# Optimization experiments

Hardware: AMD Instinct MI355X
Metric: run time of the kernel (lower is better)

## Reference

```python
import jax, jax.numpy as jnp
import numpy as np

EMB = 1024
HEADS = 16
HEAD_DIM = EMB // HEADS
FF = 4 * EMB
EPS = 1e-5


def setup_inputs() -> dict:
    key = jax.random.key(0)
    ks = jax.random.split(key, 16)
    s = 0.02
    return {
        "x": jax.random.normal(ks[0], (2, 2048, EMB), dtype=jnp.float32),
        "ln1_g": jnp.ones((EMB,), jnp.float32),
        "ln1_b": jnp.zeros((EMB,), jnp.float32),
        "Wq": jax.random.normal(ks[1], (EMB, EMB), jnp.float32) * s,
        "bq": jnp.zeros((EMB,), jnp.float32),
        "Wk": jax.random.normal(ks[2], (EMB, EMB), jnp.float32) * s,
        "bk": jnp.zeros((EMB,), jnp.float32),
        "Wv": jax.random.normal(ks[3], (EMB, EMB), jnp.float32) * s,
        "bv": jnp.zeros((EMB,), jnp.float32),
        "Wo": jax.random.normal(ks[4], (EMB, EMB), jnp.float32) * s,
        "bo": jnp.zeros((EMB,), jnp.float32),
        "ln2_g": jnp.ones((EMB,), jnp.float32),
        "ln2_b": jnp.zeros((EMB,), jnp.float32),
        "W1": jax.random.normal(ks[5], (EMB, FF), jnp.float32) * s,
        "b1": jnp.zeros((FF,), jnp.float32),
        "W2": jax.random.normal(ks[6], (FF, EMB), jnp.float32) * s,
        "b2": jnp.zeros((EMB,), jnp.float32),
    }


def _layernorm(x, g, b):
    mu = jnp.mean(x, axis=-1, keepdims=True)
    var = jnp.var(x, axis=-1, keepdims=True)
    return (x - mu) * jax.lax.rsqrt(var + EPS) * g + b


def _attention(x, Wq, bq, Wk, bk, Wv, bv, Wo, bo):
    B, T, C = x.shape
    # [B,T,C] -> [B,H,T,Dh]
    def split(y):
        return y.reshape(B, T, HEADS, HEAD_DIM).transpose(0, 2, 1, 3)
    Q = split(x @ Wq + bq)
    K = split(x @ Wk + bk)
    V = split(x @ Wv + bv)
    att = jnp.einsum("bhqd,bhkd->bhqk", Q, K) / np.sqrt(HEAD_DIM).astype(np.float32)
    causal = jnp.tril(jnp.ones((T, T), bool))
    att = jnp.where(causal, att, -jnp.inf)
    att = jax.nn.softmax(att, axis=-1)
    out = jnp.einsum("bhqk,bhkd->bhqd", att, V)
    out = out.transpose(0, 2, 1, 3).reshape(B, T, C)
    return out @ Wo + bo


def reference(x, ln1_g, ln1_b, Wq, bq, Wk, bk, Wv, bv, Wo, bo,
              ln2_g, ln2_b, W1, b1, W2, b2):
    # dropout is identity in eval mode
    x = x + _attention(_layernorm(x, ln1_g, ln1_b), Wq, bq, Wk, bk, Wv, bv, Wo, bo)
    h = _layernorm(x, ln2_g, ln2_b)
    h = jax.nn.gelu(h @ W1 + b1, approximate=False) @ W2 + b2
    return x + h
```

## Files before the change

kernel.cpp:

```cpp
#include <hip/hip_runtime.h>
#include <hip/hip_bf16.h>

typedef __attribute__((ext_vector_type(4))) float f32x4;
typedef __attribute__((ext_vector_type(8))) short bf16x8;
typedef unsigned int u32;
typedef unsigned short u16;

#define GASP __attribute__((address_space(1)))
#define LASP __attribute__((address_space(3)))

__device__ __forceinline__ u16 f2bf(float f) {
  u32 u = __float_as_uint(f);
  return (u16)((u + 0x7fffu + ((u >> 16) & 1u)) >> 16);
}

__device__ __forceinline__ void gl_lds16(const void* g, void* l) {
  __builtin_amdgcn_global_load_lds((const GASP u32*)g, (LASP u32*)l, 16, 0, 0);
}

struct CastArgs {
  const float* s[6];
  u16* d[6];
};

__global__ __launch_bounds__(256) void cast_w(CastArgs a) {
  int bid = blockIdx.x;
  int w, t, K, N, kshift;
  if (bid < 4096)      { w = bid >> 10; t = bid & 1023; K = 1024; N = 1024; kshift = 5; }
  else if (bid < 8192) { w = 4; t = bid - 4096; K = 1024; N = 4096; kshift = 5; }
  else                 { w = 5; t = bid - 8192; K = 4096; N = 1024; kshift = 7; }
  int tk = t & ((1 << kshift) - 1);
  int tn = t >> kshift;
  int k0 = tk << 5, n0 = tn << 5;
  const float* src = a.s[w];
  u16* dst = a.d[w];
  __shared__ u16 tile[32][36];
  int r = threadIdx.x >> 3, c0 = (threadIdx.x & 7) << 2;
  float4 v = *(const float4*)&src[(size_t)(k0 + r) * N + n0 + c0];
  tile[c0 + 0][r] = f2bf(v.x);
  tile[c0 + 1][r] = f2bf(v.y);
  tile[c0 + 2][r] = f2bf(v.z);
  tile[c0 + 3][r] = f2bf(v.w);
  __syncthreads();
  ushort4 o;
  o.x = tile[r][c0 + 0];
  o.y = tile[r][c0 + 1];
  o.z = tile[r][c0 + 2];
  o.w = tile[r][c0 + 3];
  *(ushort4*)&dst[(size_t)(n0 + r) * K + k0 + c0] = o;
}

__global__ __launch_bounds__(256) void ln_k(const float* __restrict__ x, const float* __restrict__ g,
                                            const float* __restrict__ b, u16* __restrict__ out) {
  int row = blockIdx.x;
  int tid = threadIdx.x;
  float4 v = *(const float4*)&x[(size_t)row * 1024 + tid * 4];
  float s = v.x + v.y + v.z + v.w;
  float ss = v.x * v.x + v.y * v.y + v.z * v.z + v.w * v.w;
#pragma unroll
  for (int o = 32; o >= 1; o >>= 1) {
    s += __shfl_xor(s, o, 64);
    ss += __shfl_xor(ss, o, 64);
  }
  __shared__ float red[8];
  int wv = tid >> 6;
  if ((tid & 63) == 0) { red[wv] = s; red[wv + 4] = ss; }
  __syncthreads();
  s = red[0] + red[1] + red[2] + red[3];
  ss = red[4] + red[5] + red[6] + red[7];
  float mu = s * (1.0f / 1024.0f);
  float var = ss * (1.0f / 1024.0f) - mu * mu;
  float rstd = rsqrtf(var + 1e-5f);
  float4 gv = *(const float4*)&g[tid * 4];
  float4 bv = *(const float4*)&b[tid * 4];
  ushort4 o4;
  o4.x = f2bf((v.x - mu) * rstd * gv.x + bv.x);
  o4.y = f2bf((v.y - mu) * rstd * gv.y + bv.y);
  o4.z = f2bf((v.z - mu) * rstd * gv.z + bv.z);
  o4.w = f2bf((v.w - mu) * rstd * gv.w + bv.w);
  *(ushort4*)&out[(size_t)row * 1024 + tid * 4] = o4;
}

template <int MODE>
__global__ __launch_bounds__(512, 2) void gemm_256(
    const u16* __restrict__ A, const u16* __restrict__ Bt,
    const float* __restrict__ bias0, const float* __restrict__ bias1, const float* __restrict__ bias2,
    void* outp, int M, int N, int K) {
  __shared__ __align__(16) u16 As[3][256 * 32];
  __shared__ __align__(16) u16 Bs[3][256 * 32];
  const int tid = threadIdx.x;
  const int w = tid >> 6, lane = tid & 63;
  const int m0 = blockIdx.y << 8, n0 = blockIdx.x << 8;

  const u16* aS[2];
  const u16* bS[2];
  char* asB = (char*)As;
  char* bsB = (char*)Bs;
#pragma unroll
  for (int i = 0; i < 2; ++i) {
    int p = w * 2048 + i * 1024 + lane * 16;
    int r = p >> 6;
    int cl = ((p >> 4) & 3) ^ ((r >> 1) & 3);
    aS[i] = A + (size_t)(m0 + r) * K + cl * 8;
    bS[i] = Bt + (size_t)(n0 + r) * K + cl * 8;
  }
  f32x4 acc[8][4];
#pragma unroll
  for (int i = 0; i < 8; ++i)
#pragma unroll
    for (int j = 0; j < 4; ++j) acc[i][j] = f32x4{0.f, 0.f, 0.f, 0.f};

  const int wr = w >> 2, wc = w & 3;
  const int qi = lane & 15;
  int aOff[8], bOff[4];
#pragma unroll
  for (int mm = 0; mm < 8; ++mm) {
    int rowa = wr * 128 + mm * 16 + qi;
    aOff[mm] = rowa * 64 + (((lane >> 4) ^ ((rowa >> 1) & 3)) << 4);
  }
#pragma unroll
  for (int nn = 0; nn < 4; ++nn) {
    int rowb = wc * 64 + nn * 16 + qi;
    bOff[nn] = rowb * 64 + (((lane >> 4) ^ ((rowb >> 1) & 3)) << 4);
  }

  gl_lds16(aS[0], asB + w * 2048);
  gl_lds16(aS[1], asB + w * 2048 + 1024);
  gl_lds16(bS[0], bsB + w * 2048);
  gl_lds16(bS[1], bsB + w * 2048 + 1024);
  if (K > 32) {
    gl_lds16(aS[0] + 32, asB + 16384 + w * 2048);
    gl_lds16(aS[1] + 32, asB + 16384 + w * 2048 + 1024);
    gl_lds16(bS[0] + 32, bsB + 16384 + w * 2048);
    gl_lds16(bS[1] + 32, bsB + 16384 + w * 2048 + 1024);
  }
  int buf = 0;
  for (int ks = 0; ks < K; ks += 32) {
    if (ks + 32 >= K) { asm volatile("s_waitcnt vmcnt(0)" ::: "memory"); }
    else              { asm volatile("s_waitcnt vmcnt(4)" ::: "memory"); }
    __builtin_amdgcn_s_barrier();
    asm volatile("" ::: "memory");
    if (ks + 64 < K) {
      const int nb = ((buf + 2) % 3) * 16384;
      gl_lds16(aS[0] + ks + 64, asB + nb + w * 2048);
      gl_lds16(aS[1] + ks + 64, asB + nb + w * 2048 + 1024);
      gl_lds16(bS[0] + ks + 64, bsB + nb + w * 2048);
      gl_lds16(bS[1] + ks + 64, bsB + nb + w * 2048 + 1024);
    }
    const int tb = buf * 16384;
    bf16x8 av[8], bv[4];
#pragma unroll
    for (int mm = 0; mm < 8; ++mm) av[mm] = *(const bf16x8*)(asB + tb + aOff[mm]);
#pragma unroll
    for (int nn = 0; nn < 4; ++nn) bv[nn] = *(const bf16x8*)(bsB + tb + bOff[nn]);
    __builtin_amdgcn_s_setprio(1);
#pragma unroll
    for (int mm = 0; mm < 8; ++mm)
#pragma unroll
      for (int nn = 0; nn < 4; ++nn)
        acc[mm][nn] = __builtin_amdgcn_mfma_f32_16x16x32_bf16(av[mm], bv[nn], acc[mm][nn], 0, 0, 0);
    __builtin_amdgcn_s_setprio(0);
    buf = buf + 1;
    if (buf == 3) buf = 0;
  }

  const int g = lane >> 4, ci = lane & 15;
#pragma unroll
  for (int mm = 0; mm < 8; ++mm) {
#pragma unroll
    for (int nn = 0; nn < 4; ++nn) {
      int colb = n0 + wc * 64 + nn * 16 + ci;
      int rowbase = m0 + wr * 128 + mm * 16 + 4 * g;
      f32x4 c = acc[mm][nn];
      if constexpr (MODE == 2) {
        int sel = colb >> 10;
        int cc = colb & 1023;
        const float* bp = sel == 0 ? bias0 : (sel == 1 ? bias1 : bias2);
        float bb = bp[cc];
        int h = cc >> 6, d = cc & 63;
        int b_ = rowbase >> 11, tt = rowbase & 2047;
        if (sel == 2) {
          u16* op = (u16*)outp + 2ull * (4096ull * 1024ull);
          ushort4 o4;
          o4.x = f2bf(c[0] + bb);
          o4.y = f2bf(c[1] + bb);
          o4.z = f2bf(c[2] + bb);
          o4.w = f2bf(c[3] + bb);
          *(ushort4*)&op[((size_t)(b_ * 16 + h) * 64 + d) * 2048 + tt] = o4;
        } else {
          float scale = (sel == 0) ? 0.125f : 1.0f;
          u16* op = (u16*)outp + (size_t)sel * (4096ull * 1024ull);
#pragma unroll
          for (int r = 0; r < 4; ++r)
            op[((size_t)(b_ * 16 + h) * 2048 + tt + r) * 64 + d] = f2bf((c[r] + bb) * scale);
        }
      } else {
        float bb = bias0[colb];
#pragma unroll
        for (int r = 0; r < 4; ++r) {
          float v = c[r] + bb;
          float gl = 0.5f * v * (1.0f + erff(v * 0.70710678118654752f));
          ((u16*)outp)[(size_t)(rowbase + r) * N + colb] = f2bf(gl);
        }
      }
    }
  }
}

__global__ __launch_bounds__(512) void gemm_sk(
    const u16* __restrict__ A, const u16* __restrict__ Bt,
    const float* __restrict__ bias0, float* __restrict__ outp,
    const float* __restrict__ res, int M, int N, int K) {
  __shared__ __align__(16) union SM {
    struct { u16 As[2][3][128 * 32]; u16 Bs[2][3][128 * 32]; } t;
    float red[16][4][4][64];
  } sm;
  const int tid = threadIdx.x;
  const int w8 = tid >> 6, lane = tid & 63;
  const int gg = w8 >> 2, wl = w8 & 3;
  const int m0 = blockIdx.y << 7, n0 = blockIdx.x << 7;

  char* asB = (char*)sm.t.As[gg];
  char* bsB = (char*)sm.t.Bs[gg];
  const u16* aS[2];
  const u16* bS[2];
#pragma unroll
  for (int i = 0; i < 2; ++i) {
    int p = wl * 2048 + i * 1024 + lane * 16;
    int r = p >> 6;
    int cl = ((p >> 4) & 3) ^ ((r >> 1) & 3);
    aS[i] = A + (size_t)(m0 + r) * K + gg * 32 + cl * 8;
    bS[i] = Bt + (size_t)(n0 + r) * K + gg * 32 + cl * 8;
  }
  f32x4 acc[4][4];
#pragma unroll
  for (int i = 0; i < 4; ++i)
#pragma unroll
    for (int j = 0; j < 4; ++j) acc[i][j] = f32x4{0.f, 0.f, 0.f, 0.f};

  const int wr = wl >> 1, wc = wl & 1;
  int aOff[4], bOff[4];
#pragma unroll
  for (int mm = 0; mm < 4; ++mm) {
    int rowa = wr * 64 + mm * 16 + (lane & 15);
    aOff[mm] = rowa * 64 + (((lane >> 4) ^ ((rowa >> 1) & 3)) << 4);
    int rowb = wc * 64 + mm * 16 + (lane & 15);
    bOff[mm] = rowb * 64 + (((lane >> 4) ^ ((rowb >> 1) & 3)) << 4);
  }

  gl_lds16(aS[0], asB + wl * 2048);
  gl_lds16(aS[1], asB + wl * 2048 + 1024);
  gl_lds16(bS[0], bsB + wl * 2048);
  gl_lds16(bS[1], bsB + wl * 2048 + 1024);
  if (K > 64) {
    gl_lds16(aS[0] + 64, asB + 8192 + wl * 2048);
    gl_lds16(aS[1] + 64, asB + 8192 + wl * 2048 + 1024);
    gl_lds16(bS[0] + 64, bsB + 8192 + wl * 2048);
    gl_lds16(bS[1] + 64, bsB + 8192 + wl * 2048 + 1024);
  }
  int buf = 0;
  for (int ks = 0; ks < K; ks += 64) {
    if (ks + 64 >= K) { asm volatile("s_waitcnt vmcnt(0)" ::: "memory"); }
    else              { asm volatile("s_waitcnt vmcnt(4)" ::: "memory"); }
    __builtin_amdgcn_s_barrier();
    asm volatile("" ::: "memory");
    if (ks + 128 < K) {
      const int nb = ((buf + 2) % 3) * 8192;
      gl_lds16(aS[0] + ks + 128, asB + nb + wl * 2048);
      gl_lds16(aS[1] + ks + 128, asB + nb + wl * 2048 + 1024);
      gl_lds16(bS[0] + ks + 128, bsB + nb + wl * 2048);
      gl_lds16(bS[1] + ks + 128, bsB + nb + wl * 2048 + 1024);
    }
    const int tb = buf * 8192;
    bf16x8 av[4], bv[4];
#pragma unroll
    for (int mm = 0; mm < 4; ++mm) av[mm] = *(const bf16x8*)(asB + tb + aOff[mm]);
#pragma unroll
    for (int nn = 0; nn < 4; ++nn) bv[nn] = *(const bf16x8*)(bsB + tb + bOff[nn]);
#pragma unroll
    for (int mm = 0; mm < 4; ++mm)
#pragma unroll
      for (int nn = 0; nn < 4; ++nn)
        acc[mm][nn] = __builtin_amdgcn_mfma_f32_16x16x32_bf16(av[mm], bv[nn], acc[mm][nn], 0, 0, 0);
    buf = buf + 1;
    if (buf == 3) buf = 0;
  }

  __syncthreads();
  if (gg == 1) {
#pragma unroll
    for (int mm = 0; mm < 4; ++mm)
#pragma unroll
      for (int nn = 0; nn < 4; ++nn)
#pragma unroll
        for (int r = 0; r < 4; ++r) sm.red[mm * 4 + nn][r][wl][lane] = acc[mm][nn][r];
  }
  __syncthreads();
  if (gg == 0) {
    const int g = lane >> 4, ci = lane & 15;
#pragma unroll
    for (int mm = 0; mm < 4; ++mm) {
#pragma unroll
      for (int nn = 0; nn < 4; ++nn) {
        int colb = n0 + wc * 64 + nn * 16 + ci;
        int rowbase = m0 + wr * 64 + mm * 16 + 4 * g;
        float bb = bias0[colb];
#pragma unroll
        for (int r = 0; r < 4; ++r) {
          size_t idx = (size_t)(rowbase + r) * N + colb;
          outp[idx] = acc[mm][nn][r] + sm.red[mm * 4 + nn][r][wl][lane] + bb + res[idx];
        }
      }
    }
  }
}

__global__ __launch_bounds__(256) void attn_k(const u16* __restrict__ Q, const u16* __restrict__ Kg,
                                              const u16* __restrict__ Vt, u16* __restrict__ O) {
  __shared__ __align__(16) u16 Ks[2][64 * 64];
  __shared__ __align__(16) u16 Vs[2][64 * 64];
  const int bx = blockIdx.x;
  const int bh = blockIdx.y;
  const int tid = threadIdx.x, w = tid >> 6, lane = tid & 63;
  const int g = lane >> 4, qi = lane & 15;
  const u16* Qb = Q + (size_t)bh * 2048 * 64;
  const u16* Kb = Kg + (size_t)bh * 2048 * 64;
  const u16* Vtb = Vt + (size_t)bh * 64 * 2048;

  const int rl8 = lane >> 3;
  const int cs = ((lane & 7) ^ rl8) * 8;
  const u16* srcK0 = Kb + (size_t)(16 * w + rl8) * 64 + cs;
  const u16* srcK1 = srcK0 + 8 * 64;
  const u16* srcV0 = Vtb + (size_t)(16 * w + rl8) * 2048 + cs;
  const u16* srcV1 = srcV0 + 8 * 2048;
  char* ksB = (char*)Ks;
  char* vsB = (char*)Vs;
  const int dstOff = w * 2048 + lane * 16;

  int koff[4][2], voff[4][2];
#pragma unroll
  for (int t = 0; t < 4; ++t) {
    int row = 16 * t + qi;
#pragma unroll
    for (int h = 0; h < 2; ++h) koff[t][h] = row * 128 + (((4 * h + g) ^ (qi & 7)) << 4);
#pragma unroll
    for (int kt = 0; kt < 2; ++kt) voff[t][kt] = row * 128 + (((4 * kt + g) ^ (qi & 7)) << 4);
  }

  const int b_ = bh >> 4, hh = bh & 15;
  u32* Ou = (u32*)O;

  for (int job = 0; job < 2; ++job) {
    const int qt = job ? bx : 31 - bx;
    const int qrow = qt * 64 + w * 16 + qi;

    bf16x8 qf[2];
#pragma unroll
    for (int h = 0; h < 2; ++h)
      qf[h] = *(const bf16x8*)(Qb + (size_t)qrow * 64 + h * 32 + g * 8);

    f32x4 acc[4];
#pragma unroll
    for (int dt = 0; dt < 4; ++dt) acc[dt] = f32x4{0.f, 0.f, 0.f, 0.f};
    float m = -1e30f, lsum = 0.0f;

    __syncthreads();
    gl_lds16(srcK0, ksB + dstOff);
    gl_lds16(srcK1, ksB + dstOff + 1024);
    gl_lds16(srcV0, vsB + dstOff);
    gl_lds16(srcV1, vsB + dstOff + 1024);

    int buf = 0;
    for (int s = 0; s <= qt; ++s) {
      __syncthreads();
      if (s < qt) {
        int nb = buf ^ 1;
        gl_lds16(srcK0 + (size_t)(s + 1) * 4096, ksB + nb * 8192 + dstOff);
        gl_lds16(srcK1 + (size_t)(s + 1) * 4096, ksB + nb * 8192 + dstOff + 1024);
        gl_lds16(srcV0 + (size_t)(s + 1) * 64, vsB + nb * 8192 + dstOff);
        gl_lds16(srcV1 + (size_t)(s + 1) * 64, vsB + nb * 8192 + dstOff + 1024);
      }
      const int tb = buf * 8192;
      f32x4 st[4];
      __builtin_amdgcn_s_setprio(1);
#pragma unroll
      for (int t = 0; t < 4; ++t) {
        st[t] = f32x4{0.f, 0.f, 0.f, 0.f};
#pragma unroll
        for (int h = 0; h < 2; ++h) {
          bf16x8 kf = *(const bf16x8*)(ksB + tb + koff[t][h]);
          st[t] = __builtin_amdgcn_mfma_f32_16x16x32_bf16(kf, qf[h], st[t], 0, 0, 0);
        }
      }
      __builtin_amdgcn_s_setprio(0);
      float pvv[4][4];
      float tmax = -1e30f;
      if (s == qt) {
#pragma unroll
        for (int t = 0; t < 4; ++t)
#pragma unroll
          for (int r = 0; r < 4; ++r) {
            int key = 64 * s + 16 * t + 4 * g + r;
            float sv = st[t][r];
            sv = (key <= qrow) ? sv : -1e30f;
            pvv[t][r] = sv;
            tmax = fmaxf(tmax, sv);
          }
      } else {
#pragma unroll
        for (int t = 0; t < 4; ++t)
#pragma unroll
          for (int r = 0; r < 4; ++r) {
            float sv = st[t][r];
            pvv[t][r] = sv;
            tmax = fmaxf(tmax, sv);
          }
      }
      tmax = fmaxf(tmax, __shfl_xor(tmax, 16, 64));
      tmax = fmaxf(tmax, __shfl_xor(tmax, 32, 64));
      float mn = fmaxf(m, tmax);
      float corr = __expf(m - mn);
      float tsum = 0.f;
#pragma unroll
      for (int t = 0; t < 4; ++t)
#pragma unroll
        for (int r = 0; r < 4; ++r) {
          float e = __expf(pvv[t][r] - mn);
          pvv[t][r] = e;
          tsum += e;
        }
      tsum += __shfl_xor(tsum, 16, 64);
      tsum += __shfl_xor(tsum, 32, 64);
      lsum = lsum * corr + tsum;
      m = mn;
#pragma unroll
      for (int dt = 0; dt < 4; ++dt)
#pragma unroll
        for (int r = 0; r < 4; ++r) acc[dt][r] *= corr;
      u32 pk[4][2], ex[4][2];
#pragma unroll
      for (int t = 0; t < 4; ++t)
#pragma unroll
        for (int p = 0; p < 2; ++p) {
          u32 v = (u32)f2bf(pvv[t][2 * p]) | ((u32)f2bf(pvv[t][2 * p + 1]) << 16);
          pk[t][p] = v;
          ex[t][p] = (u32)__shfl_xor((int)v, 16, 64);
        }
      const bool ge = (g & 1) == 0;
      const bool G0 = (g >> 1) == 0;
      const bool innr = (g == 0) || (g == 3);
      u32 mm_[4][4];
#pragma unroll
      for (int t = 0; t < 4; ++t) {
        mm_[t][0] = ge ? pk[t][0] : ex[t][0];
        mm_[t][1] = ge ? pk[t][1] : ex[t][1];
        mm_[t][2] = ge ? ex[t][0] : pk[t][0];
        mm_[t][3] = ge ? ex[t][1] : pk[t][1];
      }
      union Frag { u32 u[4]; bf16x8 v; } f0, f1;
#pragma unroll
      for (int i = 0; i < 4; ++i) {
        u32 sel0 = G0 ? mm_[1][i] : mm_[0][i];
        u32 sel1 = G0 ? mm_[3][i] : mm_[2][i];
        u32 sw0 = (u32)__shfl_xor((int)sel0, 32, 64);
        u32 sw1 = (u32)__shfl_xor((int)sel1, 32, 64);
        u32 own0 = G0 ? mm_[0][i] : mm_[1][i];
        u32 own1 = G0 ? mm_[2][i] : mm_[3][i];
        f0.u[i] = innr ? own0 : sw0;
        f1.u[i] = innr ? own1 : sw1;
      }
      __builtin_amdgcn_s_setprio(1);
#pragma unroll
      for (int dt = 0; dt < 4; ++dt) {
        bf16x8 vfa = *(const bf16x8*)(vsB + tb + voff[dt][0]);
        acc[dt] = __builtin_amdgcn_mfma_f32_16x16x32_bf16(vfa, f0.v, acc[dt], 0, 0, 0);
        bf16x8 vfb = *(const bf16x8*)(vsB + tb + voff[dt][1]);
        acc[dt] = __builtin_amdgcn_mfma_f32_16x16x32_bf16(vfb, f1.v, acc[dt], 0, 0, 0);
      }
      __builtin_amdgcn_s_setprio(0);
      buf ^= 1;
    }

    float rl = 1.0f / lsum;
    size_t rowq = (size_t)(b_ * 2048 + qrow);
#pragma unroll
    for (int dt = 0; dt < 4; ++dt) {
#pragma unroll
      for (int rp = 0; rp < 2; ++rp) {
        u16 lo = f2bf(acc[dt][rp * 2] * rl);
        u16 hi = f2bf(acc[dt][rp * 2 + 1] * rl);
        u32 pkd = (u32)lo | ((u32)hi << 16);
        size_t off = rowq * 1024 + hh * 64 + dt * 16 + 4 * g + rp * 2;
        Ou[off >> 1] = pkd;
      }
    }
  }
}

extern "C" void kernel_launch(void* const* d_in, const int* in_sizes, int n_in,
                              void* d_out, int out_size, void* d_ws, size_t ws_size,
                              hipStream_t stream) {
  const float* x    = (const float*)d_in[0];
  const float* ln1g = (const float*)d_in[1];
  const float* ln1b = (const float*)d_in[2];
  const float* Wq   = (const float*)d_in[3];
  const float* bq   = (const float*)d_in[4];
  const float* Wk   = (const float*)d_in[5];
  const float* bk   = (const float*)d_in[6];
  const float* Wv   = (const float*)d_in[7];
  const float* bv   = (const float*)d_in[8];
  const float* Wo   = (const float*)d_in[9];
  const float* bo   = (const float*)d_in[10];
  const float* ln2g = (const float*)d_in[11];
  const float* ln2b = (const float*)d_in[12];
  const float* W1   = (const float*)d_in[13];
  const float* b1   = (const float*)d_in[14];
  const float* W2   = (const float*)d_in[15];
  const float* b2   = (const float*)d_in[16];

  char* ws = (char*)d_ws;
  const size_t MB = 1ull << 20;
  u16* WqT = (u16*)(ws + 0 * MB);
  u16* WkT = (u16*)(ws + 2 * MB);
  u16* WvT = (u16*)(ws + 4 * MB);
  u16* WoT = (u16*)(ws + 6 * MB);
  u16* W1T = (u16*)(ws + 8 * MB);
  u16* W2T = (u16*)(ws + 16 * MB);
  u16* XN  = (u16*)(ws + 24 * MB);
  u16* Qb  = (u16*)(ws + 32 * MB);
  u16* Kb  = (u16*)(ws + 40 * MB);
  u16* Vtb = (u16*)(ws + 48 * MB);
  u16* Ob  = (u16*)(ws + 56 * MB);
  u16* Gb  = (u16*)(ws + 32 * MB);

  CastArgs ca;
  ca.s[0] = Wq; ca.s[1] = Wk; ca.s[2] = Wv; ca.s[3] = Wo; ca.s[4] = W1; ca.s[5] = W2;
  ca.d[0] = WqT; ca.d[1] = WkT; ca.d[2] = WvT; ca.d[3] = WoT; ca.d[4] = W1T; ca.d[5] = W2T;
  cast_w<<<12288, 256, 0, stream>>>(ca);

  ln_k<<<4096, 256, 0, stream>>>(x, ln1g, ln1b, XN);

  gemm_256<2><<<dim3(12, 16), 512, 0, stream>>>(XN, WqT, bq, bk, bv, Qb, 4096, 3072, 1024);

  attn_k<<<dim3(16, 32), 256, 0, stream>>>(Qb, Kb, Vtb, Ob);

  gemm_sk<<<dim3(8, 32), 512, 0, stream>>>(Ob, WoT, bo, (float*)d_out, x, 4096, 1024, 1024);

  ln_k<<<4096, 256, 0, stream>>>((const float*)d_out, ln2g, ln2b, XN);

  gemm_256<3><<<dim3(16, 16), 512, 0, stream>>>(XN, W1T, b1, nullptr, nullptr, Gb, 4096, 4096, 1024);

  gemm_sk<<<dim3(8, 32), 512, 0, stream>>>(Gb, W2T, b2, (float*)d_out, (const float*)d_out, 4096, 1024, 4096);
}
```

Measured before the change: 257.8 us.

## Enlarge attention query tile, add lazy softmax rescale, XCD-aware GEMM block swizzle

The attention kernel now uses 512 threads and 128-query tiles, so each K/V tile loaded into LDS serves eight waves, halving K/V traffic per query. Waves whose rows lie entirely before a KV tile skip it. The online softmax only rescales when the running max grows by more than a threshold, and bf16 packing uses the hardware v_cvt_pk_bf16_f32 instruction. GEMM blocks are remapped across the 8 XCDs so that neighbouring tiles share L2. Larger blocks halve the attention grid to 256 workgroups, which may lower occupancy and leave waves idle on the causal diagonal.

```diff
diff --git a/kernel.cpp b/kernel.cpp
--- a/kernel.cpp
+++ b/kernel.cpp
@@ -12,6 +12,12 @@
 __device__ __forceinline__ u16 f2bf(float f) {
   u32 u = __float_as_uint(f);
   return (u16)((u + 0x7fffu + ((u >> 16) & 1u)) >> 16);
+}
+
+__device__ __forceinline__ u32 cvtpk(float lo, float hi) {
+  u32 r;
+  asm("v_cvt_pk_bf16_f32 %0, %1, %2" : "=v"(r) : "v"(lo), "v"(hi));
+  return r;
 }
 
 __device__ __forceinline__ void gl_lds16(const void* g, void* l) {
@@ -85,12 +91,15 @@
 __global__ __launch_bounds__(512, 2) void gemm_256(
     const u16* __restrict__ A, const u16* __restrict__ Bt,
     const float* __restrict__ bias0, const float* __restrict__ bias1, const float* __restrict__ bias2,
-    void* outp, int M, int N, int K) {
+    void* outp, int nbx, int M, int N, int K) {
   __shared__ __align__(16) u16 As[3][256 * 32];
   __shared__ __align__(16) u16 Bs[3][256 * 32];
   const int tid = threadIdx.x;
   const int w = tid >> 6, lane = tid & 63;
-  const int m0 = blockIdx.y << 8, n0 = blockIdx.x << 8;
+  const int nwg = gridDim.x;
+  const int cpx = nwg >> 3;
+  const int sb = (blockIdx.x & 7) * cpx + (blockIdx.x >> 3);
+  const int m0 = (sb / nbx) << 8, n0 = (sb % nbx) << 8;
 
   const u16* aS[2];
   const u16* bS[2];
@@ -315,7 +324,7 @@
   }
 }
 
-__global__ __launch_bounds__(256) void attn_k(const u16* __restrict__ Q, const u16* __restrict__ Kg,
+__global__ __launch_bounds__(512) void attn_k(const u16* __restrict__ Q, const u16* __restrict__ Kg,
                                               const u16* __restrict__ Vt, u16* __restrict__ O) {
   __shared__ __align__(16) u16 Ks[2][64 * 64];
   __shared__ __align__(16) u16 Vs[2][64 * 64];
@@ -327,15 +336,13 @@
   const u16* Kb = Kg + (size_t)bh * 2048 * 64;
   const u16* Vtb = Vt + (size_t)bh * 64 * 2048;
 
-  const int rl8 = lane >> 3;
-  const int cs = ((lane & 7) ^ rl8) * 8;
-  const u16* srcK0 = Kb + (size_t)(16 * w + rl8) * 64 + cs;
-  const u16* srcK1 = srcK0 + 8 * 64;
-  const u16* srcV0 = Vtb + (size_t)(16 * w + rl8) * 2048 + cs;
-  const u16* srcV1 = srcV0 + 8 * 2048;
+  const int rS = tid >> 3, cS = tid & 7;
+  const int csw = (cS ^ (rS & 7)) * 8;
+  const u16* srcK = Kb + (size_t)rS * 64 + csw;
+  const u16* srcV = Vtb + (size_t)rS * 2048 + csw;
   char* ksB = (char*)Ks;
   char* vsB = (char*)Vs;
-  const int dstOff = w * 2048 + lane * 16;
+  const int dstOff = tid * 16;
 
   int koff[4][2], voff[4][2];
 #pragma unroll
@@ -351,8 +358,9 @@
   u32* Ou = (u32*)O;
 
   for (int job = 0; job < 2; ++job) {
-    const int qt = job ? bx : 31 - bx;
-    const int qrow = qt * 64 + w * 16 + qi;
+    const int qt = job ? bx : 15 - bx;
+    const int qrow = qt * 128 + w * 16 + qi;
+    const int qmaxw = qt * 128 + w * 16 + 15;
 
     bf16x8 qf[2];
 #pragma unroll
@@ -365,119 +373,122 @@
     float m = -1e30f, lsum = 0.0f;
 
     __syncthreads();
-    gl_lds16(srcK0, ksB + dstOff);
-    gl_lds16(srcK1, ksB + dstOff + 1024);
-    gl_lds16(srcV0, vsB + dstOff);
-    gl_lds16(srcV1, vsB + dstOff + 1024);
-
+    gl_lds16(srcK, ksB + dstOff);
+    gl_lds16(srcV, vsB + dstOff);
+
+    const int nsteps = 2 * qt + 2;
     int buf = 0;
-    for (int s = 0; s <= qt; ++s) {
+    for (int s = 0; s < nsteps; ++s) {
       __syncthreads();
-      if (s < qt) {
+      if (s + 1 < nsteps) {
         int nb = buf ^ 1;
-        gl_lds16(srcK0 + (size_t)(s + 1) * 4096, ksB + nb * 8192 + dstOff);
-        gl_lds16(srcK1 + (size_t)(s + 1) * 4096, ksB + nb * 8192 + dstOff + 1024);
-        gl_lds16(srcV0 + (size_t)(s + 1) * 64, vsB + nb * 8192 + dstOff);
-        gl_lds16(srcV1 + (size_t)(s + 1) * 64, vsB + nb * 8192 + dstOff + 1024);
+        gl_lds16(srcK + (size_t)(s + 1) * 4096, ksB + nb * 8192 + dstOff);
+        gl_lds16(srcV + (size_t)(s + 1) * 64, vsB + nb * 8192 + dstOff);
       }
-      const int tb = buf * 8192;
-      f32x4 st[4];
-      __builtin_amdgcn_s_setprio(1);
-#pragma unroll
-      for (int t = 0; t < 4; ++t) {
-        st[t] = f32x4{0.f, 0.f, 0.f, 0.f};
-#pragma unroll
-        for (int h = 0; h < 2; ++h) {
-          bf16x8 kf = *(const bf16x8*)(ksB + tb + koff[t][h]);
-          st[t] = __builtin_amdgcn_mfma_f32_16x16x32_bf16(kf, qf[h], st[t], 0, 0, 0);
-        }
+      const int kv0 = s * 64;
+      if (kv0 <= qmaxw) {
+        const int tb = buf * 8192;
+        f32x4 st[4];
+        __builtin_amdgcn_s_setprio(1);
+#pragma unroll
+        for (int t = 0; t < 4; ++t) {
+          st[t] = f32x4{0.f, 0.f, 0.f, 0.f};
+#pragma unroll
+          for (int h = 0; h < 2; ++h) {
+            bf16x8 kf = *(const bf16x8*)(ksB + tb + koff[t][h]);
+            st[t] = __builtin_amdgcn_mfma_f32_16x16x32_bf16(kf, qf[h], st[t], 0, 0, 0);
+          }
+        }
+        __builtin_amdgcn_s_setprio(0);
+        float pvv[4][4];
+        float tmax = -1e30f;
+        if (kv0 + 63 > qmaxw) {
+#pragma unroll
+          for (int t = 0; t < 4; ++t)
+#pragma unroll
+            for (int r = 0; r < 4; ++r) {
+              int key = kv0 + 16 * t + 4 * g + r;
+              float sv = st[t][r];
+              sv = (key <= qrow) ? sv : -1e30f;
+              pvv[t][r] = sv;
+              tmax = fmaxf(tmax, sv);
+            }
+        } else {
+#pragma unroll
+          for (int t = 0; t < 4; ++t)
+#pragma unroll
+            for (int r = 0; r < 4; ++r) {
+              float sv = st[t][r];
+              pvv[t][r] = sv;
+              tmax = fmaxf(tmax, sv);
+            }
+        }
+        tmax = fmaxf(tmax, __shfl_xor(tmax, 16, 64));
+        tmax = fmaxf(tmax, __shfl_xor(tmax, 32, 64));
+        if (!__all(tmax <= m + 8.0f)) {
+          float mn = fmaxf(m, tmax);
+          float corr = __expf(m - mn);
+          lsum *= corr;
+#pragma unroll
+          for (int dt = 0; dt < 4; ++dt)
+#pragma unroll
+            for (int r = 0; r < 4; ++r) acc[dt][r] *= corr;
+          m = mn;
+        }
+        float tsum = 0.f;
+#pragma unroll
+        for (int t = 0; t < 4; ++t)
+#pragma unroll
+          for (int r = 0; r < 4; ++r) {
+            float e = __expf(pvv[t][r] - m);
+            pvv[t][r] = e;
+            tsum += e;
+          }
+        tsum += __shfl_xor(tsum, 16, 64);
+        tsum += __shfl_xor(tsum, 32, 64);
+        lsum += tsum;
+        u32 pk[4][2], ex[4][2];
+#pragma unroll
+        for (int t = 0; t < 4; ++t)
+#pragma unroll
+          for (int p = 0; p < 2; ++p) {
+            u32 v = cvtpk(pvv[t][2 * p], pvv[t][2 * p + 1]);
+            pk[t][p] = v;
+            ex[t][p] = (u32)__shfl_xor((int)v, 16, 64);
+          }
+        const bool ge = (g & 1) == 0;
+        const bool G0 = (g >> 1) == 0;
+        const bool innr = (g == 0) || (g == 3);
+        u32 mm_[4][4];
+#pragma unroll
+        for (int t = 0; t < 4; ++t) {
+          mm_[t][0] = ge ? pk[t][0] : ex[t][0];
+          mm_[t][1] = ge ? pk[t][1] : ex[t][1];
+          mm_[t][2] = ge ? ex[t][0] : pk[t][0];
+          mm_[t][3] = ge ? ex[t][1] : pk[t][1];
+        }
+        union Frag { u32 u[4]; bf16x8 v; } f0, f1;
+#pragma unroll
+        for (int i = 0; i < 4; ++i) {
+          u32 sel0 = G0 ? mm_[1][i] : mm_[0][i];
+          u32 sel1 = G0 ? mm_[3][i] : mm_[2][i];
+          u32 sw0 = (u32)__shfl_xor((int)sel0, 32, 64);
+          u32 sw1 = (u32)__shfl_xor((int)sel1, 32, 64);
+          u32 own0 = G0 ? mm_[0][i] : mm_[1][i];
+          u32 own1 = G0 ? mm_[2][i] : mm_[3][i];
+          f0.u[i] = innr ? own0 : sw0;
+          f1.u[i] = innr ? own1 : sw1;
+        }
+        __builtin_amdgcn_s_setprio(1);
+#pragma unroll
+        for (int dt = 0; dt < 4; ++dt) {
+          bf16x8 vfa = *(const bf16x8*)(vsB + tb + voff[dt][0]);
+          acc[dt] = __builtin_amdgcn_mfma_f32_16x16x32_bf16(vfa, f0.v, acc[dt], 0, 0, 0);
+          bf16x8 vfb = *(const bf16x8*)(vsB + tb + voff[dt][1]);
+          acc[dt] = __builtin_amdgcn_mfma_f32_16x16x32_bf16(vfb, f1.v, acc[dt], 0, 0, 0);
+        }
+        __builtin_amdgcn_s_setprio(0);
       }
-      __builtin_amdgcn_s_setprio(0);
-      float pvv[4][4];
-      float tmax = -1e30f;
-      if (s == qt) {
-#pragma unroll
-        for (int t = 0; t < 4; ++t)
-#pragma unroll
-          for (int r = 0; r < 4; ++r) {
-            int key = 64 * s + 16 * t + 4 * g + r;
-            float sv = st[t][r];
-            sv = (key <= qrow) ? sv : -1e30f;
-            pvv[t][r] = sv;
-            tmax = fmaxf(tmax, sv);
-          }
-      } else {
-#pragma unroll
-        for (int t = 0; t < 4; ++t)
-#pragma unroll
-          for (int r = 0; r < 4; ++r) {
-            float sv = st[t][r];
-            pvv[t][r] = sv;
-            tmax = fmaxf(tmax, sv);
-          }
-      }
-      tmax = fmaxf(tmax, __shfl_xor(tmax, 16, 64));
-      tmax = fmaxf(tmax, __shfl_xor(tmax, 32, 64));
-      float mn = fmaxf(m, tmax);
-      float corr = __expf(m - mn);
-      float tsum = 0.f;
-#pragma unroll
-      for (int t = 0; t < 4; ++t)
-#pragma unroll
-        for (int r = 0; r < 4; ++r) {
-          float e = __expf(pvv[t][r] - mn);
-          pvv[t][r] = e;
-          tsum += e;
-        }
-      tsum += __shfl_xor(tsum, 16, 64);
-      tsum += __shfl_xor(tsum, 32, 64);
-      lsum = lsum * corr + tsum;
-      m = mn;
-#pragma unroll
-      for (int dt = 0; dt < 4; ++dt)
-#pragma unroll
-        for (int r = 0; r < 4; ++r) acc[dt][r] *= corr;
-      u32 pk[4][2], ex[4][2];
-#pragma unroll
-      for (int t = 0; t < 4; ++t)
-#pragma unroll
-        for (int p = 0; p < 2; ++p) {
-          u32 v = (u32)f2bf(pvv[t][2 * p]) | ((u32)f2bf(pvv[t][2 * p + 1]) << 16);
-          pk[t][p] = v;
-          ex[t][p] = (u32)__shfl_xor((int)v, 16, 64);
-        }
-      const bool ge = (g & 1) == 0;
-      const bool G0 = (g >> 1) == 0;
-      const bool innr = (g == 0) || (g == 3);
-      u32 mm_[4][4];
-#pragma unroll
-      for (int t = 0; t < 4; ++t) {
-        mm_[t][0] = ge ? pk[t][0] : ex[t][0];
-        mm_[t][1] = ge ? pk[t][1] : ex[t][1];
-        mm_[t][2] = ge ? ex[t][0] : pk[t][0];
-        mm_[t][3] = ge ? ex[t][1] : pk[t][1];
-      }
-      union Frag { u32 u[4]; bf16x8 v; } f0, f1;
-#pragma unroll
-      for (int i = 0; i < 4; ++i) {
-        u32 sel0 = G0 ? mm_[1][i] : mm_[0][i];
-        u32 sel1 = G0 ? mm_[3][i] : mm_[2][i];
-        u32 sw0 = (u32)__shfl_xor((int)sel0, 32, 64);
-        u32 sw1 = (u32)__shfl_xor((int)sel1, 32, 64);
-        u32 own0 = G0 ? mm_[0][i] : mm_[1][i];
-        u32 own1 = G0 ? mm_[2][i] : mm_[3][i];
-        f0.u[i] = innr ? own0 : sw0;
-        f1.u[i] = innr ? own1 : sw1;
-      }
-      __builtin_amdgcn_s_setprio(1);
-#pragma unroll
-      for (int dt = 0; dt < 4; ++dt) {
-        bf16x8 vfa = *(const bf16x8*)(vsB + tb + voff[dt][0]);
-        acc[dt] = __builtin_amdgcn_mfma_f32_16x16x32_bf16(vfa, f0.v, acc[dt], 0, 0, 0);
-        bf16x8 vfb = *(const bf16x8*)(vsB + tb + voff[dt][1]);
-        acc[dt] = __builtin_amdgcn_mfma_f32_16x16x32_bf16(vfb, f1.v, acc[dt], 0, 0, 0);
-      }
-      __builtin_amdgcn_s_setprio(0);
       buf ^= 1;
     }
 
@@ -487,9 +498,7 @@
     for (int dt = 0; dt < 4; ++dt) {
 #pragma unroll
       for (int rp = 0; rp < 2; ++rp) {
-        u16 lo = f2bf(acc[dt][rp * 2] * rl);
-        u16 hi = f2bf(acc[dt][rp * 2 + 1] * rl);
-        u32 pkd = (u32)lo | ((u32)hi << 16);
+        u32 pkd = cvtpk(acc[dt][rp * 2] * rl, acc[dt][rp * 2 + 1] * rl);
         size_t off = rowq * 1024 + hh * 64 + dt * 16 + 4 * g + rp * 2;
         Ou[off >> 1] = pkd;
       }
@@ -540,15 +549,15 @@
 
   ln_k<<<4096, 256, 0, stream>>>(x, ln1g, ln1b, XN);
 
-  gemm_256<2><<<dim3(12, 16), 512, 0, stream>>>(XN, WqT, bq, bk, bv, Qb, 4096, 3072, 1024);
-
-  attn_k<<<dim3(16, 32), 256, 0, stream>>>(Qb, Kb, Vtb, Ob);
+  gemm_256<2><<<12 * 16, 512, 0, stream>>>(XN, WqT, bq, bk, bv, Qb, 12, 4096, 3072, 1024);
+
+  attn_k<<<dim3(8, 32), 512, 0, stream>>>(Qb, Kb, Vtb, Ob);
 
   gemm_sk<<<dim3(8, 32), 512, 0, stream>>>(Ob, WoT, bo, (float*)d_out, x, 4096, 1024, 1024);
 
   ln_k<<<4096, 256, 0, stream>>>((const float*)d_out, ln2g, ln2b, XN);
 
-  gemm_256<3><<<dim3(16, 16), 512, 0, stream>>>(XN, W1T, b1, nullptr, nullptr, Gb, 4096, 4096, 1024);
+  gemm_256<3><<<16 * 16, 512, 0, stream>>>(XN, W1T, b1, nullptr, nullptr, Gb, 16, 4096, 4096, 1024);
 
   gemm_sk<<<dim3(8, 32), 512, 0, stream>>>(Gb, W2T, b2, (float*)d_out, (const float*)d_out, 4096, 1024, 4096);
 }
```

New measurement: 252.1 us. 2.2% less time.
